# Performance work log

Hardware: AMD Instinct MI355X
Metric: run time of the kernel (lower is better)

The kernel has to match this reference:

```python
import jax, jax.numpy as jnp
import numpy as np

INPUT_SIZE = 128
HIDDEN = 512
OUTPUT = 10
NUM_LAYERS = 6
B, T = 64, 256


def setup_inputs() -> dict:
    key = jax.random.key(0)
    ks = jax.random.split(key, 2 + 4 * NUM_LAYERS + 2)
    k = 1.0 / np.sqrt(HIDDEN)  # torch LSTM init scale
    inp = {"x": jax.random.normal(ks[0], (B, T, INPUT_SIZE), dtype=jnp.float32)}
    # layer 0 input-to-hidden has input dim INPUT_SIZE; layers 1..5 have HIDDEN
    inp["W_ih0"] = jax.random.uniform(ks[1], (4 * HIDDEN, INPUT_SIZE), minval=-k, maxval=k)
    inp["W_ih_rest"] = jax.random.uniform(ks[2], (NUM_LAYERS - 1, 4 * HIDDEN, HIDDEN), minval=-k, maxval=k)
    inp["W_hh"] = jax.random.uniform(ks[3], (NUM_LAYERS, 4 * HIDDEN, HIDDEN), minval=-k, maxval=k)
    inp["b_ih"] = jax.random.uniform(ks[4], (NUM_LAYERS, 4 * HIDDEN), minval=-k, maxval=k)
    inp["b_hh"] = jax.random.uniform(ks[5], (NUM_LAYERS, 4 * HIDDEN), minval=-k, maxval=k)
    inp["fc_w"] = jax.random.uniform(ks[6], (OUTPUT, HIDDEN), minval=-k, maxval=k)
    inp["fc_b"] = jax.random.uniform(ks[7], (OUTPUT,), minval=-k, maxval=k)
    return inp


def _lstm_layer(x, W_ih, W_hh, b_ih, b_hh):
    # x: [B, T, D_in] -> h sequence [B, T, H]. Torch gate order: i, f, g, o.
    Bsz = x.shape[0]
    H = W_hh.shape[1]
    # Precompute all input projections in one big GEMM: [B, T, 4H]
    xp = jnp.einsum('btd,gd->btg', x, W_ih) + b_ih + b_hh
    xp_t = jnp.swapaxes(xp, 0, 1)  # [T, B, 4H] for scan over time

    def step(carry, xt):
        h, c = carry
        gates = xt + h @ W_hh.T  # [B, 4H]
        i, f, g, o = jnp.split(gates, 4, axis=-1)
        i = jax.nn.sigmoid(i)
        f = jax.nn.sigmoid(f)
        g = jnp.tanh(g)
        o = jax.nn.sigmoid(o)
        c = f * c + i * g
        h = o * jnp.tanh(c)
        return (h, c), h

    h0 = jnp.zeros((Bsz, H), dtype=x.dtype)
    c0 = jnp.zeros((Bsz, H), dtype=x.dtype)
    _, hs = jax.lax.scan(step, (h0, c0), xp_t)
    return jnp.swapaxes(hs, 0, 1)  # [B, T, H]


def reference(x, W_ih0, W_ih_rest, W_hh, b_ih, b_hh, fc_w, fc_b):
    out = _lstm_layer(x, W_ih0, W_hh[0], b_ih[0], b_hh[0])
    for l in range(1, NUM_LAYERS):
        out = _lstm_layer(out, W_ih_rest[l - 1], W_hh[l], b_ih[l], b_hh[l])
    # final FC on last timestep
    return out[:, -1, :] @ fc_w.T + fc_b
```

## Files before the change

kernel.cpp:

```cpp
#include <hip/hip_runtime.h>

#define B 64
#define T 256
#define H 512
#define G4 2048
#define D0 128
#define NL 6
#define NBLK_P 192
#define SKEW 2
#define GTOT (T + SKEW * (NL - 1))
#define FSTRIDE 16
#define RD 8
#define HSTRA 584
#define HSTRB 520
#define GSTR 36

typedef float f32x4 __attribute__((ext_vector_type(4)));
typedef float f32x16 __attribute__((ext_vector_type(16)));
typedef _Float16 h16x8 __attribute__((ext_vector_type(8)));

#define CLOAD(dst, p) \
  asm volatile("global_load_dwordx4 %0, %1, off sc0 sc1" : "=&v"(dst) : "v"(p))
#define VMWAIT do { asm volatile("s_waitcnt vmcnt(0)" ::: "memory"); \
                    __builtin_amdgcn_sched_barrier(0); } while (0)

__global__ void __launch_bounds__(1024, 4) lstm_pipe(
    const float* __restrict__ x,
    const float* __restrict__ Wih0, const float* __restrict__ WihR,
    const float* __restrict__ Whh,
    const float* __restrict__ bih, const float* __restrict__ bhh,
    unsigned short* __restrict__ ring, float* __restrict__ h5,
    unsigned* __restrict__ flags)
{
  __shared__ unsigned short h_sA[64 * HSTRA];
  __shared__ unsigned short h_sB[64 * HSTRB];
  float* const g_par = (float*)h_sA;

  const int tid  = threadIdx.x;
  const int lane = tid & 63;
  const int wl   = __builtin_amdgcn_readfirstlane(tid >> 6);
  const int ks   = wl & 3;
  const int rt   = (wl >> 2) >> 1;
  const int bt   = (wl >> 2) & 1;
  const int blk  = (int)blockIdx.x;
  const int l    = blk >> 5;
  const int jb   = blk & 31;
  const int j0   = jb * 16;
  const int Kin  = (l == 0) ? D0 : H;
  const int KA4  = Kin >> 2;
  const int FA   = KA4 >> 4;

  const float* WihA = (l == 0) ? Wih0 : (WihR + (size_t)(l - 1) * G4 * H);
  const float* WhhA = Whh + (size_t)l * G4 * H;

  h16x8 aA[8], aB[8];
  {
    const int ri   = rt * 32 + (lane & 31);
    const int grow = (ri >> 4) * H + j0 + (ri & 15);
    const float* wihRow = WihA + (size_t)grow * Kin;
    const float* whhRow = WhhA + (size_t)grow * H;
    const int klane = (lane >> 5) * 8;
#pragma unroll
    for (int m = 0; m < 8; ++m) {
      h16x8 fa = {};
      if (m < FA) {
        const float* src = wihRow + ks * KA4 + m * 16 + klane;
        f32x4 v0 = *(const f32x4*)src, v1 = *(const f32x4*)(src + 4);
        fa[0] = (_Float16)v0.x; fa[1] = (_Float16)v0.y;
        fa[2] = (_Float16)v0.z; fa[3] = (_Float16)v0.w;
        fa[4] = (_Float16)v1.x; fa[5] = (_Float16)v1.y;
        fa[6] = (_Float16)v1.z; fa[7] = (_Float16)v1.w;
      }
      aA[m] = fa;
      const float* srb = whhRow + ks * 128 + m * 16 + klane;
      f32x4 w0 = *(const f32x4*)srb, w1 = *(const f32x4*)(srb + 4);
      h16x8 fb;
      fb[0] = (_Float16)w0.x; fb[1] = (_Float16)w0.y;
      fb[2] = (_Float16)w0.z; fb[3] = (_Float16)w0.w;
      fb[4] = (_Float16)w1.x; fb[5] = (_Float16)w1.y;
      fb[6] = (_Float16)w1.z; fb[7] = (_Float16)w1.w;
      aB[m] = fb;
    }
  }

  const int pb = tid >> 4, pcj = tid & 15;
  float bias4[4];
#pragma unroll
  for (int gi = 0; gi < 4; ++gi) {
    int grow = gi * H + j0 + pcj;
    bias4[gi] = bih[(size_t)l * G4 + grow] + bhh[(size_t)l * G4 + grow];
  }

  const int koff = (lane >> 5) * 8;
  float creg = 0.f;

  for (int g = 0; g < GTOT; ++g) {
    const int t = g - SKEW * l;
    const bool active = (t >= 0) && (t < T);

    if (active) {
      if (g > 0) {
        if (tid < 32) {
          if (l > 0) {
            unsigned* f = &flags[((l - 1) * 32 + tid) * FSTRIDE];
            while ((int)__hip_atomic_load(f, __ATOMIC_RELAXED,
                                          __HIP_MEMORY_SCOPE_AGENT) < g - 1)
              __builtin_amdgcn_s_sleep(1);
          }
        } else if (tid < 64) {
          if (l < NL - 1) {
            unsigned* f = &flags[((l + 1) * 32 + (tid - 32)) * FSTRIDE];
            while ((int)__hip_atomic_load(f, __ATOMIC_RELAXED,
                                          __HIP_MEMORY_SCOPE_AGENT) < g - 5)
              __builtin_amdgcn_s_sleep(1);
          }
        }
        __syncthreads();
      }

      if (l == 0) {
        const int row = tid >> 4, u = tid & 15;
        const float* xr = x + ((size_t)row * T + t) * D0 + u * 8;
        f32x4 v0 = *(const f32x4*)xr, v1 = *(const f32x4*)(xr + 4);
        h16x8 f;
        f[0] = (_Float16)v0.x; f[1] = (_Float16)v0.y;
        f[2] = (_Float16)v0.z; f[3] = (_Float16)v0.w;
        f[4] = (_Float16)v1.x; f[5] = (_Float16)v1.y;
        f[6] = (_Float16)v1.z; f[7] = (_Float16)v1.w;
        *(h16x8*)&h_sA[row * HSTRA + u * 8] = f;
      } else {
        const unsigned short* rgA =
            ring + ((size_t)(l - 1) * RD + (t & (RD - 1))) * (B * H);
        f32x4 rr[4];
#pragma unroll
        for (int i = 0; i < 4; ++i) {
          int uu = tid + 1024 * i;
          CLOAD(rr[i], rgA + (size_t)(uu >> 6) * H + (uu & 63) * 8);
        }
        VMWAIT;
#pragma unroll
        for (int i = 0; i < 4; ++i) {
          int uu = tid + 1024 * i;
          *(f32x4*)&h_sA[(uu >> 6) * HSTRA + (uu & 63) * 8] = rr[i];
        }
      }
      __syncthreads();

      f32x16 accv = {};
      {
        const unsigned short* ba =
            &h_sA[(bt * 32 + (lane & 31)) * HSTRA + ks * KA4 + koff];
#pragma unroll
        for (int m = 0; m < 8; ++m) {
          if (m < FA) {
            h16x8 b8 = *(const h16x8*)(ba + m * 16);
            accv = __builtin_amdgcn_mfma_f32_32x32x16_f16(aA[m], b8, accv, 0, 0, 0);
          }
        }
      }

      if (t > 0 && tid < 32) {
        unsigned* f = &flags[(l * 32 + tid) * FSTRIDE];
        while ((int)__hip_atomic_load(f, __ATOMIC_RELAXED,
                                      __HIP_MEMORY_SCOPE_AGENT) < g)
          __builtin_amdgcn_s_sleep(1);
      }
      __syncthreads();

      if (t > 0) {
        const unsigned short* rgB =
            ring + ((size_t)l * RD + ((t - 1) & (RD - 1))) * (B * H);
        f32x4 rr[4];
#pragma unroll
        for (int i = 0; i < 4; ++i) {
          int uu = tid + 1024 * i;
          CLOAD(rr[i], rgB + (size_t)(uu >> 6) * H + (uu & 63) * 8);
        }
        VMWAIT;
#pragma unroll
        for (int i = 0; i < 4; ++i) {
          int uu = tid + 1024 * i;
          *(f32x4*)&h_sB[(uu >> 6) * HSTRB + (uu & 63) * 8] = rr[i];
        }
      }
      __syncthreads();

      if (t > 0) {
        const unsigned short* bb =
            &h_sB[(bt * 32 + (lane & 31)) * HSTRB + ks * 128 + koff];
#pragma unroll
        for (int m = 0; m < 8; ++m) {
          h16x8 b8 = *(const h16x8*)(bb + m * 16);
          accv = __builtin_amdgcn_mfma_f32_32x32x16_f16(aB[m], b8, accv, 0, 0, 0);
        }
      }

      {
        float* gp = g_par +
            (size_t)((ks * 4 + (rt * 2 + bt)) * 32 + (lane & 31)) * GSTR +
            4 * (lane >> 5);
#pragma unroll
        for (int q = 0; q < 4; ++q) {
          f32x4 tv;
          tv.x = accv[4 * q];     tv.y = accv[4 * q + 1];
          tv.z = accv[4 * q + 2]; tv.w = accv[4 * q + 3];
          *(f32x4*)&gp[8 * q] = tv;
        }
      }
      __syncthreads();

      {
        float gt[4];
#pragma unroll
        for (int gi = 0; gi < 4; ++gi) {
          int rowL = gi * 16 + pcj;
          int tile = (rowL >> 5) * 2 + (pb >> 5);
          int rL   = rowL & 31;
          float s = bias4[gi];
#pragma unroll
          for (int ksi = 0; ksi < 4; ++ksi)
            s += g_par[(size_t)((ksi * 4 + tile) * 32 + (pb & 31)) * GSTR + rL];
          gt[gi] = s;
        }
        float iv = 1.f / (1.f + expf(-gt[0]));
        float fv = 1.f / (1.f + expf(-gt[1]));
        float gv = tanhf(gt[2]);
        float ov = 1.f / (1.f + expf(-gt[3]));
        creg = fv * creg + iv * gv;
        float hv = ov * tanhf(creg);
        _Float16 hf = (_Float16)hv;
        __hip_atomic_store(
            &ring[((size_t)l * RD + (t & (RD - 1))) * (B * H) + pb * H + j0 + pcj],
            __builtin_bit_cast(unsigned short, hf),
            __ATOMIC_RELAXED, __HIP_MEMORY_SCOPE_AGENT);
        if (l == NL - 1 && t == T - 1)
          h5[pb * H + j0 + pcj] = hv;
      }
      __syncthreads();
    }

    if (tid == 0)
      __hip_atomic_store(&flags[blk * FSTRIDE], (unsigned)(g + 1),
                         __ATOMIC_RELAXED, __HIP_MEMORY_SCOPE_AGENT);
  }
}

__global__ void __launch_bounds__(640) fc_kernel(
    const float* __restrict__ h5, const float* __restrict__ w,
    const float* __restrict__ bias, float* __restrict__ out)
{
  int tid = threadIdx.x;
  if (tid >= 640) return;
  int b = tid / 10, o = tid - b * 10;
  const float* yr = h5 + (size_t)b * H;
  const float* wr = w + (size_t)o * H;
  float acc = bias[o];
  for (int k = 0; k < H; ++k) acc = fmaf(yr[k], wr[k], acc);
  out[b * 10 + o] = acc;
}

extern "C" void kernel_launch(void* const* d_in, const int* in_sizes, int n_in,
                              void* d_out, int out_size, void* d_ws,
                              size_t ws_size, hipStream_t stream)
{
  const float* x    = (const float*)d_in[0];
  const float* Wih0 = (const float*)d_in[1];
  const float* WihR = (const float*)d_in[2];
  const float* Whh  = (const float*)d_in[3];
  const float* bih  = (const float*)d_in[4];
  const float* bhh  = (const float*)d_in[5];
  const float* fcw  = (const float*)d_in[6];
  const float* fcb  = (const float*)d_in[7];
  float* out = (float*)d_out;

  unsigned* flags = (unsigned*)d_ws;
  unsigned short* ring = (unsigned short*)((char*)d_ws + 16384);
  float* h5buf = (float*)((char*)d_ws + 16384 + (size_t)NL * RD * B * H * 2);

  hipMemsetAsync(d_ws, 0, 16384, stream);

  lstm_pipe<<<NBLK_P, 1024, 0, stream>>>(x, Wih0, WihR, Whh, bih, bhh,
                                         ring, h5buf, flags);
  fc_kernel<<<1, 640, 0, stream>>>(h5buf, fcw, fcb, out);
}
```

Before: 1.246 ms.

## Use full-length per-timestep hidden buffer to drop backpressure waits and uncached loads

When the workspace is large enough, the hidden-state ring is replaced by a buffer with one slot per timestep for every layer, so no slot is ever overwritten. This lets each layer skip waiting on the downstream layer's progress flags. It also lets reads use ordinary cached vector loads instead of sc0/sc1 loads followed by a full vmcnt wait. The cost is a much larger workspace footprint and worse cache locality for the hidden states. Correctness now relies on plain loads never seeing stale cached lines for data written by other blocks, for example lines left over from an earlier launch; otherwise the original ring path is used.

Result: faster. 1.181 ms (-5.2%).

```diff
diff --git a/kernel.cpp b/kernel.cpp
--- a/kernel.cpp
+++ b/kernel.cpp
@@ -24,6 +24,7 @@
 #define VMWAIT do { asm volatile("s_waitcnt vmcnt(0)" ::: "memory"); \
                     __builtin_amdgcn_sched_barrier(0); } while (0)
 
+template<int L2C>
 __global__ void __launch_bounds__(1024, 4) lstm_pipe(
     const float* __restrict__ x,
     const float* __restrict__ Wih0, const float* __restrict__ WihR,
@@ -107,7 +108,7 @@
                                           __HIP_MEMORY_SCOPE_AGENT) < g - 1)
               __builtin_amdgcn_s_sleep(1);
           }
-        } else if (tid < 64) {
+        } else if (!L2C && tid < 64) {
           if (l < NL - 1) {
             unsigned* f = &flags[((l + 1) * 32 + (tid - 32)) * FSTRIDE];
             while ((int)__hip_atomic_load(f, __ATOMIC_RELAXED,
@@ -129,15 +130,24 @@
         f[6] = (_Float16)v1.z; f[7] = (_Float16)v1.w;
         *(h16x8*)&h_sA[row * HSTRA + u * 8] = f;
       } else {
+        const int slotA = L2C ? t : (t & (RD - 1));
         const unsigned short* rgA =
-            ring + ((size_t)(l - 1) * RD + (t & (RD - 1))) * (B * H);
+            ring + ((size_t)(l - 1) * (L2C ? T : RD) + slotA) * (B * H);
         f32x4 rr[4];
-#pragma unroll
-        for (int i = 0; i < 4; ++i) {
-          int uu = tid + 1024 * i;
-          CLOAD(rr[i], rgA + (size_t)(uu >> 6) * H + (uu & 63) * 8);
-        }
-        VMWAIT;
+        if (L2C) {
+#pragma unroll
+          for (int i = 0; i < 4; ++i) {
+            int uu = tid + 1024 * i;
+            rr[i] = *(const f32x4*)(rgA + (size_t)(uu >> 6) * H + (uu & 63) * 8);
+          }
+        } else {
+#pragma unroll
+          for (int i = 0; i < 4; ++i) {
+            int uu = tid + 1024 * i;
+            CLOAD(rr[i], rgA + (size_t)(uu >> 6) * H + (uu & 63) * 8);
+          }
+          VMWAIT;
+        }
 #pragma unroll
         for (int i = 0; i < 4; ++i) {
           int uu = tid + 1024 * i;
@@ -168,15 +178,24 @@
       __syncthreads();
 
       if (t > 0) {
+        const int slotB = L2C ? (t - 1) : ((t - 1) & (RD - 1));
         const unsigned short* rgB =
-            ring + ((size_t)l * RD + ((t - 1) & (RD - 1))) * (B * H);
+            ring + ((size_t)l * (L2C ? T : RD) + slotB) * (B * H);
         f32x4 rr[4];
-#pragma unroll
-        for (int i = 0; i < 4; ++i) {
-          int uu = tid + 1024 * i;
-          CLOAD(rr[i], rgB + (size_t)(uu >> 6) * H + (uu & 63) * 8);
-        }
-        VMWAIT;
+        if (L2C) {
+#pragma unroll
+          for (int i = 0; i < 4; ++i) {
+            int uu = tid + 1024 * i;
+            rr[i] = *(const f32x4*)(rgB + (size_t)(uu >> 6) * H + (uu & 63) * 8);
+          }
+        } else {
+#pragma unroll
+          for (int i = 0; i < 4; ++i) {
+            int uu = tid + 1024 * i;
+            CLOAD(rr[i], rgB + (size_t)(uu >> 6) * H + (uu & 63) * 8);
+          }
+          VMWAIT;
+        }
 #pragma unroll
         for (int i = 0; i < 4; ++i) {
           int uu = tid + 1024 * i;
@@ -229,8 +248,9 @@
         creg = fv * creg + iv * gv;
         float hv = ov * tanhf(creg);
         _Float16 hf = (_Float16)hv;
+        const int slotW = L2C ? t : (t & (RD - 1));
         __hip_atomic_store(
-            &ring[((size_t)l * RD + (t & (RD - 1))) * (B * H) + pb * H + j0 + pcj],
+            &ring[((size_t)l * (L2C ? T : RD) + slotW) * (B * H) + pb * H + j0 + pcj],
             __builtin_bit_cast(unsigned short, hf),
             __ATOMIC_RELAXED, __HIP_MEMORY_SCOPE_AGENT);
         if (l == NL - 1 && t == T - 1)
@@ -275,11 +295,22 @@
 
   unsigned* flags = (unsigned*)d_ws;
   unsigned short* ring = (unsigned short*)((char*)d_ws + 16384);
-  float* h5buf = (float*)((char*)d_ws + 16384 + (size_t)NL * RD * B * H * 2);
+
+  const size_t ringFull = (size_t)NL * T * B * H * 2;
+  const size_t ringFall = (size_t)NL * RD * B * H * 2;
+  const size_t needFull = 16384 + ringFull + (size_t)B * H * 4;
 
   hipMemsetAsync(d_ws, 0, 16384, stream);
 
-  lstm_pipe<<<NBLK_P, 1024, 0, stream>>>(x, Wih0, WihR, Whh, bih, bhh,
-                                         ring, h5buf, flags);
-  fc_kernel<<<1, 640, 0, stream>>>(h5buf, fcw, fcb, out);
+  if (ws_size >= needFull) {
+    float* h5buf = (float*)((char*)d_ws + 16384 + ringFull);
+    lstm_pipe<1><<<NBLK_P, 1024, 0, stream>>>(x, Wih0, WihR, Whh, bih, bhh,
+                                              ring, h5buf, flags);
+    fc_kernel<<<1, 640, 0, stream>>>(h5buf, fcw, fcb, out);
+  } else {
+    float* h5buf = (float*)((char*)d_ws + 16384 + ringFall);
+    lstm_pipe<0><<<NBLK_P, 1024, 0, stream>>>(x, Wih0, WihR, Whh, bih, bhh,
+                                              ring, h5buf, flags);
+    fc_kernel<<<1, 640, 0, stream>>>(h5buf, fcw, fcb, out);
+  }
 }
```

## Use full-length history buffer and per-wave flag waits instead of block barriers

Applied to the files above, without the earlier changes.

Replaces the 8-deep ring with a buffer holding every timestep per layer, so the producer no longer has to wait for the downstream layer before overwriting, and that back-pressure wait is removed. Each 32-thread group now polls only the one producer block whose column slice it loads, instead of one wave polling all producers and then synchronising the whole block. The coherent sc0/sc1 inline-asm loads become ordinary vector loads. This trades a much larger workspace for fewer barriers and finer-grained dependencies, but plain loads may hit stale cached data, since the flag polling uses relaxed atomics with no acquire fence.

Result: slower. 1.856 ms (+48.9%).

```diff
diff --git a/kernel.cpp b/kernel.cpp
--- a/kernel.cpp
+++ b/kernel.cpp
@@ -10,7 +10,6 @@
 #define SKEW 2
 #define GTOT (T + SKEW * (NL - 1))
 #define FSTRIDE 16
-#define RD 8
 #define HSTRA 584
 #define HSTRB 520
 #define GSTR 36
@@ -18,11 +17,6 @@
 typedef float f32x4 __attribute__((ext_vector_type(4)));
 typedef float f32x16 __attribute__((ext_vector_type(16)));
 typedef _Float16 h16x8 __attribute__((ext_vector_type(8)));
-
-#define CLOAD(dst, p) \
-  asm volatile("global_load_dwordx4 %0, %1, off sc0 sc1" : "=&v"(dst) : "v"(p))
-#define VMWAIT do { asm volatile("s_waitcnt vmcnt(0)" ::: "memory"); \
-                    __builtin_amdgcn_sched_barrier(0); } while (0)
 
 __global__ void __launch_bounds__(1024, 4) lstm_pipe(
     const float* __restrict__ x,
@@ -92,6 +86,7 @@
   }
 
   const int koff = (lane >> 5) * 8;
+  const int grp = tid >> 5, li = tid & 31;
   float creg = 0.f;
 
   for (int g = 0; g < GTOT; ++g) {
@@ -99,25 +94,6 @@
     const bool active = (t >= 0) && (t < T);
 
     if (active) {
-      if (g > 0) {
-        if (tid < 32) {
-          if (l > 0) {
-            unsigned* f = &flags[((l - 1) * 32 + tid) * FSTRIDE];
-            while ((int)__hip_atomic_load(f, __ATOMIC_RELAXED,
-                                          __HIP_MEMORY_SCOPE_AGENT) < g - 1)
-              __builtin_amdgcn_s_sleep(1);
-          }
-        } else if (tid < 64) {
-          if (l < NL - 1) {
-            unsigned* f = &flags[((l + 1) * 32 + (tid - 32)) * FSTRIDE];
-            while ((int)__hip_atomic_load(f, __ATOMIC_RELAXED,
-                                          __HIP_MEMORY_SCOPE_AGENT) < g - 5)
-              __builtin_amdgcn_s_sleep(1);
-          }
-        }
-        __syncthreads();
-      }
-
       if (l == 0) {
         const int row = tid >> 4, u = tid & 15;
         const float* xr = x + ((size_t)row * T + t) * D0 + u * 8;
@@ -129,20 +105,20 @@
         f[6] = (_Float16)v1.z; f[7] = (_Float16)v1.w;
         *(h16x8*)&h_sA[row * HSTRA + u * 8] = f;
       } else {
+        unsigned* fp = &flags[((l - 1) * 32 + grp) * FSTRIDE];
+        while ((int)__hip_atomic_load(fp, __ATOMIC_RELAXED,
+                                      __HIP_MEMORY_SCOPE_AGENT) < g - 1)
+          __builtin_amdgcn_s_sleep(1);
         const unsigned short* rgA =
-            ring + ((size_t)(l - 1) * RD + (t & (RD - 1))) * (B * H);
-        f32x4 rr[4];
-#pragma unroll
-        for (int i = 0; i < 4; ++i) {
-          int uu = tid + 1024 * i;
-          CLOAD(rr[i], rgA + (size_t)(uu >> 6) * H + (uu & 63) * 8);
-        }
-        VMWAIT;
-#pragma unroll
-        for (int i = 0; i < 4; ++i) {
-          int uu = tid + 1024 * i;
-          *(f32x4*)&h_sA[(uu >> 6) * HSTRA + (uu & 63) * 8] = rr[i];
-        }
+            ring + ((size_t)(l - 1) * T + t) * (B * H) + grp * 16;
+        const unsigned short* s0 = rgA + (size_t)li * H;
+        const unsigned short* s1 = rgA + (size_t)(li + 32) * H;
+        f32x4 a0 = *(const f32x4*)s0, a1 = *(const f32x4*)(s0 + 8);
+        f32x4 b0 = *(const f32x4*)s1, b1 = *(const f32x4*)(s1 + 8);
+        *(f32x4*)&h_sA[li * HSTRA + grp * 16]            = a0;
+        *(f32x4*)&h_sA[li * HSTRA + grp * 16 + 8]        = a1;
+        *(f32x4*)&h_sA[(li + 32) * HSTRA + grp * 16]     = b0;
+        *(f32x4*)&h_sA[(li + 32) * HSTRA + grp * 16 + 8] = b1;
       }
       __syncthreads();
 
@@ -159,29 +135,21 @@
         }
       }
 
-      if (t > 0 && tid < 32) {
-        unsigned* f = &flags[(l * 32 + tid) * FSTRIDE];
-        while ((int)__hip_atomic_load(f, __ATOMIC_RELAXED,
+      if (t > 0) {
+        unsigned* fp = &flags[(l * 32 + grp) * FSTRIDE];
+        while ((int)__hip_atomic_load(fp, __ATOMIC_RELAXED,
                                       __HIP_MEMORY_SCOPE_AGENT) < g)
           __builtin_amdgcn_s_sleep(1);
-      }
-      __syncthreads();
-
-      if (t > 0) {
         const unsigned short* rgB =
-            ring + ((size_t)l * RD + ((t - 1) & (RD - 1))) * (B * H);
-        f32x4 rr[4];
-#pragma unroll
-        for (int i = 0; i < 4; ++i) {
-          int uu = tid + 1024 * i;
-          CLOAD(rr[i], rgB + (size_t)(uu >> 6) * H + (uu & 63) * 8);
-        }
-        VMWAIT;
-#pragma unroll
-        for (int i = 0; i < 4; ++i) {
-          int uu = tid + 1024 * i;
-          *(f32x4*)&h_sB[(uu >> 6) * HSTRB + (uu & 63) * 8] = rr[i];
-        }
+            ring + ((size_t)l * T + (t - 1)) * (B * H) + grp * 16;
+        const unsigned short* s0 = rgB + (size_t)li * H;
+        const unsigned short* s1 = rgB + (size_t)(li + 32) * H;
+        f32x4 a0 = *(const f32x4*)s0, a1 = *(const f32x4*)(s0 + 8);
+        f32x4 b0 = *(const f32x4*)s1, b1 = *(const f32x4*)(s1 + 8);
+        *(f32x4*)&h_sB[li * HSTRB + grp * 16]            = a0;
+        *(f32x4*)&h_sB[li * HSTRB + grp * 16 + 8]        = a1;
+        *(f32x4*)&h_sB[(li + 32) * HSTRB + grp * 16]     = b0;
+        *(f32x4*)&h_sB[(li + 32) * HSTRB + grp * 16 + 8] = b1;
       }
       __syncthreads();
 
@@ -230,7 +198,7 @@
         float hv = ov * tanhf(creg);
         _Float16 hf = (_Float16)hv;
         __hip_atomic_store(
-            &ring[((size_t)l * RD + (t & (RD - 1))) * (B * H) + pb * H + j0 + pcj],
+            &ring[((size_t)l * T + t) * (B * H) + pb * H + j0 + pcj],
             __builtin_bit_cast(unsigned short, hf),
             __ATOMIC_RELAXED, __HIP_MEMORY_SCOPE_AGENT);
         if (l == NL - 1 && t == T - 1)
@@ -275,7 +243,8 @@
 
   unsigned* flags = (unsigned*)d_ws;
   unsigned short* ring = (unsigned short*)((char*)d_ws + 16384);
-  float* h5buf = (float*)((char*)d_ws + 16384 + (size_t)NL * RD * B * H * 2);
+  const size_t ringFull = (size_t)NL * T * B * H * 2;
+  float* h5buf = (float*)((char*)d_ws + 16384 + ringFull);
 
   hipMemsetAsync(d_ws, 0, 16384, stream);
 
```

## Prefetch next-step input projection off the critical path with a full-length ring

Applied to the files above, without the earlier changes.

Replaces the 8-slot ring buffer with a full T-length history per layer. This removes the back-pressure wait on the downstream layer, and with it the need for cache-bypassing loads. For layers above 0, the input-projection MFMAs for step t+1 are computed after the flag publish of step t, so only the recurrent h@W_hh part stays on the critical path. Layer 0 stages its x input in a separate shared buffer. Ring loads become plain loads instead of sc0/sc1 bypass loads. This relies on the relaxed atomic flags still ordering the data correctly. The launch bound's min-blocks hint is lowered and the workspace footprint grows to about 100MB.

Result: slower. 1.471 ms (+18.0%).

```diff
diff --git a/kernel.cpp b/kernel.cpp
--- a/kernel.cpp
+++ b/kernel.cpp
@@ -10,21 +10,16 @@
 #define SKEW 2
 #define GTOT (T + SKEW * (NL - 1))
 #define FSTRIDE 16
-#define RD 8
 #define HSTRA 584
 #define HSTRB 520
+#define XSTR  136
 #define GSTR 36
 
 typedef float f32x4 __attribute__((ext_vector_type(4)));
 typedef float f32x16 __attribute__((ext_vector_type(16)));
 typedef _Float16 h16x8 __attribute__((ext_vector_type(8)));
 
-#define CLOAD(dst, p) \
-  asm volatile("global_load_dwordx4 %0, %1, off sc0 sc1" : "=&v"(dst) : "v"(p))
-#define VMWAIT do { asm volatile("s_waitcnt vmcnt(0)" ::: "memory"); \
-                    __builtin_amdgcn_sched_barrier(0); } while (0)
-
-__global__ void __launch_bounds__(1024, 4) lstm_pipe(
+__global__ void __launch_bounds__(1024, 2) lstm_pipe(
     const float* __restrict__ x,
     const float* __restrict__ Wih0, const float* __restrict__ WihR,
     const float* __restrict__ Whh,
@@ -34,6 +29,7 @@
 {
   __shared__ unsigned short h_sA[64 * HSTRA];
   __shared__ unsigned short h_sB[64 * HSTRB];
+  __shared__ unsigned short x_s [64 * XSTR];
   float* const g_par = (float*)h_sA;
 
   const int tid  = threadIdx.x;
@@ -93,32 +89,46 @@
 
   const int koff = (lane >> 5) * 8;
   float creg = 0.f;
+  f32x16 accv = {};
 
   for (int g = 0; g < GTOT; ++g) {
-    const int t = g - SKEW * l;
-    const bool active = (t >= 0) && (t < T);
-
-    if (active) {
-      if (g > 0) {
-        if (tid < 32) {
-          if (l > 0) {
-            unsigned* f = &flags[((l - 1) * 32 + tid) * FSTRIDE];
-            while ((int)__hip_atomic_load(f, __ATOMIC_RELAXED,
-                                          __HIP_MEMORY_SCOPE_AGENT) < g - 1)
-              __builtin_amdgcn_s_sleep(1);
+    const int t  = g - SKEW * l;
+    const int tN = t + 1;
+    const bool act = (t >= 0) && (t < T);
+    const bool pfA = (l > 0) && (tN >= 0) && (tN < T);
+
+    if (act || pfA) {
+      {
+        const bool ns = act && (t > 0);
+        if ((ns || pfA) && tid < 32) {
+          unsigned* fs = &flags[(l * 32 + tid) * FSTRIDE];
+          unsigned* fu = pfA ? &flags[((l - 1) * 32 + tid) * FSTRIDE]
+                             : (unsigned*)0;
+          for (;;) {
+            int ok = 1;
+            if (ns) ok &= ((int)__hip_atomic_load(fs, __ATOMIC_RELAXED,
+                                __HIP_MEMORY_SCOPE_AGENT) >= g);
+            if (fu) ok &= ((int)__hip_atomic_load(fu, __ATOMIC_RELAXED,
+                                __HIP_MEMORY_SCOPE_AGENT) >= g);
+            if (ok) break;
+            __builtin_amdgcn_s_sleep(1);
           }
-        } else if (tid < 64) {
-          if (l < NL - 1) {
-            unsigned* f = &flags[((l + 1) * 32 + (tid - 32)) * FSTRIDE];
-            while ((int)__hip_atomic_load(f, __ATOMIC_RELAXED,
-                                          __HIP_MEMORY_SCOPE_AGENT) < g - 5)
-              __builtin_amdgcn_s_sleep(1);
-          }
-        }
-        __syncthreads();
-      }
-
-      if (l == 0) {
+        }
+      }
+      __syncthreads();
+
+      f32x4 pf[4];
+      if (pfA) {
+        const unsigned short* rgA =
+            ring + ((size_t)(l - 1) * T + tN) * (B * H);
+#pragma unroll
+        for (int i = 0; i < 4; ++i) {
+          int uu = tid + 1024 * i;
+          pf[i] = *(const f32x4*)(rgA + (size_t)(uu >> 6) * H + (uu & 63) * 8);
+        }
+      }
+
+      if (act && l == 0) {
         const int row = tid >> 4, u = tid & 15;
         const float* xr = x + ((size_t)row * T + t) * D0 + u * 8;
         f32x4 v0 = *(const f32x4*)xr, v1 = *(const f32x4*)(xr + 4);
@@ -127,75 +137,46 @@
         f[2] = (_Float16)v0.z; f[3] = (_Float16)v0.w;
         f[4] = (_Float16)v1.x; f[5] = (_Float16)v1.y;
         f[6] = (_Float16)v1.z; f[7] = (_Float16)v1.w;
-        *(h16x8*)&h_sA[row * HSTRA + u * 8] = f;
-      } else {
-        const unsigned short* rgA =
-            ring + ((size_t)(l - 1) * RD + (t & (RD - 1))) * (B * H);
-        f32x4 rr[4];
-#pragma unroll
-        for (int i = 0; i < 4; ++i) {
-          int uu = tid + 1024 * i;
-          CLOAD(rr[i], rgA + (size_t)(uu >> 6) * H + (uu & 63) * 8);
-        }
-        VMWAIT;
-#pragma unroll
-        for (int i = 0; i < 4; ++i) {
-          int uu = tid + 1024 * i;
-          *(f32x4*)&h_sA[(uu >> 6) * HSTRA + (uu & 63) * 8] = rr[i];
-        }
-      }
-      __syncthreads();
-
-      f32x16 accv = {};
-      {
-        const unsigned short* ba =
-            &h_sA[(bt * 32 + (lane & 31)) * HSTRA + ks * KA4 + koff];
-#pragma unroll
-        for (int m = 0; m < 8; ++m) {
-          if (m < FA) {
+        *(h16x8*)&x_s[row * XSTR + u * 8] = f;
+      }
+
+      if (act && t > 0) {
+        const unsigned short* rgB =
+            ring + ((size_t)l * T + (t - 1)) * (B * H);
+        f32x4 rb[4];
+#pragma unroll
+        for (int i = 0; i < 4; ++i) {
+          int uu = tid + 1024 * i;
+          rb[i] = *(const f32x4*)(rgB + (size_t)(uu >> 6) * H + (uu & 63) * 8);
+        }
+#pragma unroll
+        for (int i = 0; i < 4; ++i) {
+          int uu = tid + 1024 * i;
+          *(f32x4*)&h_sB[(uu >> 6) * HSTRB + (uu & 63) * 8] = rb[i];
+        }
+      }
+      __syncthreads();
+
+      if (act) {
+        if (l == 0) {
+          accv = (f32x16){};
+          const unsigned short* ba =
+              &x_s[(bt * 32 + (lane & 31)) * XSTR + ks * KA4 + koff];
+#pragma unroll
+          for (int m = 0; m < 2; ++m) {
             h16x8 b8 = *(const h16x8*)(ba + m * 16);
             accv = __builtin_amdgcn_mfma_f32_32x32x16_f16(aA[m], b8, accv, 0, 0, 0);
           }
         }
-      }
-
-      if (t > 0 && tid < 32) {
-        unsigned* f = &flags[(l * 32 + tid) * FSTRIDE];
-        while ((int)__hip_atomic_load(f, __ATOMIC_RELAXED,
-                                      __HIP_MEMORY_SCOPE_AGENT) < g)
-          __builtin_amdgcn_s_sleep(1);
-      }
-      __syncthreads();
-
-      if (t > 0) {
-        const unsigned short* rgB =
-            ring + ((size_t)l * RD + ((t - 1) & (RD - 1))) * (B * H);
-        f32x4 rr[4];
-#pragma unroll
-        for (int i = 0; i < 4; ++i) {
-          int uu = tid + 1024 * i;
-          CLOAD(rr[i], rgB + (size_t)(uu >> 6) * H + (uu & 63) * 8);
-        }
-        VMWAIT;
-#pragma unroll
-        for (int i = 0; i < 4; ++i) {
-          int uu = tid + 1024 * i;
-          *(f32x4*)&h_sB[(uu >> 6) * HSTRB + (uu & 63) * 8] = rr[i];
-        }
-      }
-      __syncthreads();
-
-      if (t > 0) {
-        const unsigned short* bb =
-            &h_sB[(bt * 32 + (lane & 31)) * HSTRB + ks * 128 + koff];
-#pragma unroll
-        for (int m = 0; m < 8; ++m) {
-          h16x8 b8 = *(const h16x8*)(bb + m * 16);
-          accv = __builtin_amdgcn_mfma_f32_32x32x16_f16(aB[m], b8, accv, 0, 0, 0);
-        }
-      }
-
-      {
+        if (t > 0) {
+          const unsigned short* bb =
+              &h_sB[(bt * 32 + (lane & 31)) * HSTRB + ks * 128 + koff];
+#pragma unroll
+          for (int m = 0; m < 8; ++m) {
+            h16x8 b8 = *(const h16x8*)(bb + m * 16);
+            accv = __builtin_amdgcn_mfma_f32_32x32x16_f16(aB[m], b8, accv, 0, 0, 0);
+          }
+        }
         float* gp = g_par +
             (size_t)((ks * 4 + (rt * 2 + bt)) * 32 + (lane & 31)) * GSTR +
             4 * (lane >> 5);
@@ -209,7 +190,7 @@
       }
       __syncthreads();
 
-      {
+      if (act) {
         float gt[4];
 #pragma unroll
         for (int gi = 0; gi < 4; ++gi) {
@@ -230,18 +211,38 @@
         float hv = ov * tanhf(creg);
         _Float16 hf = (_Float16)hv;
         __hip_atomic_store(
-            &ring[((size_t)l * RD + (t & (RD - 1))) * (B * H) + pb * H + j0 + pcj],
+            &ring[((size_t)l * T + t) * (B * H) + pb * H + j0 + pcj],
             __builtin_bit_cast(unsigned short, hf),
             __ATOMIC_RELAXED, __HIP_MEMORY_SCOPE_AGENT);
         if (l == NL - 1 && t == T - 1)
           h5[pb * H + j0 + pcj] = hv;
       }
       __syncthreads();
+
+      if (pfA) {
+#pragma unroll
+        for (int i = 0; i < 4; ++i) {
+          int uu = tid + 1024 * i;
+          *(f32x4*)&h_sA[(uu >> 6) * HSTRA + (uu & 63) * 8] = pf[i];
+        }
+      }
     }
 
     if (tid == 0)
       __hip_atomic_store(&flags[blk * FSTRIDE], (unsigned)(g + 1),
                          __ATOMIC_RELAXED, __HIP_MEMORY_SCOPE_AGENT);
+
+    if (pfA) {
+      __syncthreads();
+      accv = (f32x16){};
+      const unsigned short* ba =
+          &h_sA[(bt * 32 + (lane & 31)) * HSTRA + ks * 128 + koff];
+#pragma unroll
+      for (int m = 0; m < 8; ++m) {
+        h16x8 b8 = *(const h16x8*)(ba + m * 16);
+        accv = __builtin_amdgcn_mfma_f32_32x32x16_f16(aA[m], b8, accv, 0, 0, 0);
+      }
+    }
   }
 }
 
@@ -275,7 +276,8 @@
 
   unsigned* flags = (unsigned*)d_ws;
   unsigned short* ring = (unsigned short*)((char*)d_ws + 16384);
-  float* h5buf = (float*)((char*)d_ws + 16384 + (size_t)NL * RD * B * H * 2);
+  const size_t ringFull = (size_t)NL * T * B * H * 2;
+  float* h5buf = (float*)((char*)d_ws + 16384 + ringFull);
 
   hipMemsetAsync(d_ws, 0, 16384, stream);
 
```
